# Kernel tuning notes

Hardware: AMD Instinct MI355X
Metric: run time of the kernel (lower is better)

## Reference

```python
import jax, jax.numpy as jnp
import numpy as np

B, N, D = 8, 1024, 512
H = 8
DH = D // H
EPS_DIST = 1e-8
EPS_LN = 1e-5


def _layer_norm(x, gamma, beta):
    mu = jnp.mean(x, axis=-1, keepdims=True)
    var = jnp.mean((x - mu) ** 2, axis=-1, keepdims=True)
    return (x - mu) * jax.lax.rsqrt(var + EPS_LN) * gamma + beta


def setup_inputs() -> dict:
    key = jax.random.key(0)
    ks = jax.random.split(key, 6)
    scale = 1.0 / np.sqrt(D)
    inp = {
        "x": jax.random.normal(ks[0], (B, N, D), dtype=jnp.float32),
        "Wq": jax.random.normal(ks[1], (D, D), dtype=jnp.float32) * scale,
        "Wk": jax.random.normal(ks[2], (D, D), dtype=jnp.float32) * scale,
        "Wv": jax.random.normal(ks[3], (D, D), dtype=jnp.float32) * scale,
        "Wo": jax.random.normal(ks[4], (D, D), dtype=jnp.float32) * scale,
        "bq": jnp.zeros((D,), jnp.float32),
        "bk": jnp.zeros((D,), jnp.float32),
        "bv": jnp.zeros((D,), jnp.float32),
        "bo": jnp.zeros((D,), jnp.float32),
        "ln1_g": jnp.ones((D,), jnp.float32),
        "ln1_b": jnp.zeros((D,), jnp.float32),
        "ln2_g": jnp.ones((D,), jnp.float32),
        "ln2_b": jnp.zeros((D,), jnp.float32),
    }
    return inp


def reference(x, Wq, bq, Wk, bk, Wv, bv, Wo, bo, ln1_g, ln1_b, ln2_g, ln2_b):
    residual = x
    h = _layer_norm(x, ln1_g, ln1_b)  # pre-norm

    def heads(t):
        # [B,N,D] -> [B,H,N,DH]
        return t.reshape(B, N, H, DH).transpose(0, 2, 1, 3)

    q = heads(h @ Wq + bq)
    k = heads(h @ Wk + bk)
    v = heads(h @ Wv + bv)

    # Euclidean pairwise distance via ||q||^2 + ||k||^2 - 2 q.k expansion
    q_sq = jnp.sum(q * q, axis=-1)[..., :, None]      # [B,H,N,1]
    k_sq = jnp.sum(k * k, axis=-1)[..., None, :]      # [B,H,1,N]
    qk = jnp.einsum("bhnd,bhmd->bhnm", q, k)          # [B,H,N,N]
    d2 = jnp.maximum(q_sq + k_sq - 2.0 * qk, 0.0)
    dist = jnp.sqrt(d2 + EPS_DIST)

    # distance -> attention score: smaller distance = higher attention
    attn = jax.nn.softmax(-dist, axis=-1)             # [B,H,N,N]

    out = jnp.einsum("bhnm,bhmd->bhnd", attn, v)      # [B,H,N,DH]
    out = out.transpose(0, 2, 1, 3).reshape(B, N, D)
    out = out @ Wo + bo

    y = residual + out
    y = _layer_norm(y, ln2_g, ln2_b)
    return y
```

## Files before the change

kernel.cpp:

```cpp
#include <hip/hip_runtime.h>
#include <math.h>

typedef __attribute__((ext_vector_type(8))) short short8;
typedef __attribute__((ext_vector_type(4))) float f32x4;
typedef __attribute__((ext_vector_type(2))) unsigned uint2v;

constexpr int B  = 8;
constexpr int N  = 1024;
constexpr int D  = 512;
constexpr int H  = 8;
constexpr int DH = 64;
constexpr int M_ROWS = 8192;
constexpr float EPS_DIST = 1e-8f;
constexpr float EPS_LN   = 1e-5f;

__device__ inline unsigned short bfbits(float f) {
    union { float f; unsigned u; } v; v.f = f;
    unsigned r = v.u + 0x7fffu + ((v.u >> 16) & 1u);
    return (unsigned short)(r >> 16);
}
__device__ inline float bf2f(unsigned short s) {
    union { unsigned u; float f; } v; v.u = ((unsigned)s) << 16; return v.f;
}

__device__ inline void async_ld16(unsigned short* lds, const unsigned short* g) {
    __builtin_amdgcn_global_load_lds(
        (const __attribute__((address_space(1))) unsigned int*)(g),
        (__attribute__((address_space(3))) unsigned int*)(lds),
        16, 0, 0);
}

__global__ __launch_bounds__(256) void prep_kernel(const float* __restrict__ Wq,
                                                   const float* __restrict__ Wk,
                                                   const float* __restrict__ Wv,
                                                   const float* __restrict__ Wo,
                                                   unsigned short* __restrict__ WtAll,
                                                   const float* __restrict__ x,
                                                   const float* __restrict__ ln1_g,
                                                   const float* __restrict__ ln1_b,
                                                   unsigned short* __restrict__ h_bf) {
    const int bxg = blockIdx.x;
    if (bxg < 256) {
        int sub = bxg >> 6;
        const float* W = sub == 0 ? Wq : sub == 1 ? Wk : sub == 2 ? Wv : Wo;
        unsigned short* Wt = WtAll + (size_t)sub * 262144;
        int t = (bxg & 63) * 256 + threadIdx.x;
        int tn = t & 127, tk = t >> 7;
        int k = tk * 4, n = tn * 4;
        float4 r0 = *(const float4*)&W[(size_t)(k + 0) * 512 + n];
        float4 r1 = *(const float4*)&W[(size_t)(k + 1) * 512 + n];
        float4 r2 = *(const float4*)&W[(size_t)(k + 2) * 512 + n];
        float4 r3 = *(const float4*)&W[(size_t)(k + 3) * 512 + n];
        ushort4 c;
        c.x = bfbits(r0.x); c.y = bfbits(r1.x); c.z = bfbits(r2.x); c.w = bfbits(r3.x);
        *(ushort4*)&Wt[(size_t)(n + 0) * 512 + k] = c;
        c.x = bfbits(r0.y); c.y = bfbits(r1.y); c.z = bfbits(r2.y); c.w = bfbits(r3.y);
        *(ushort4*)&Wt[(size_t)(n + 1) * 512 + k] = c;
        c.x = bfbits(r0.z); c.y = bfbits(r1.z); c.z = bfbits(r2.z); c.w = bfbits(r3.z);
        *(ushort4*)&Wt[(size_t)(n + 2) * 512 + k] = c;
        c.x = bfbits(r0.w); c.y = bfbits(r1.w); c.z = bfbits(r2.w); c.w = bfbits(r3.w);
        *(ushort4*)&Wt[(size_t)(n + 3) * 512 + k] = c;
    } else {
        const int w = threadIdx.x >> 6, lane = threadIdx.x & 63;
        const int row = (bxg - 256) * 4 + w;
        const float4* xr = (const float4*)(x + (size_t)row * D);
        float4 a = xr[lane], b2 = xr[lane + 64];
        float s = a.x + a.y + a.z + a.w + b2.x + b2.y + b2.z + b2.w;
        #pragma unroll
        for (int o = 1; o < 64; o <<= 1) s += __shfl_xor(s, o, 64);
        const float mu = s * (1.0f / 512.0f);
        float d0 = a.x - mu, d1 = a.y - mu, d2 = a.z - mu, d3 = a.w - mu;
        float e0 = b2.x - mu, e1 = b2.y - mu, e2 = b2.z - mu, e3 = b2.w - mu;
        float vs = d0*d0 + d1*d1 + d2*d2 + d3*d3 + e0*e0 + e1*e1 + e2*e2 + e3*e3;
        #pragma unroll
        for (int o = 1; o < 64; o <<= 1) vs += __shfl_xor(vs, o, 64);
        const float rstd = rsqrtf(vs * (1.0f / 512.0f) + EPS_LN);
        const float4* g4 = (const float4*)ln1_g;
        const float4* b4 = (const float4*)ln1_b;
        float4 ga = g4[lane], gb = g4[lane + 64];
        float4 ba = b4[lane], bb = b4[lane + 64];
        ushort4 u;
        u.x = bfbits(d0 * rstd * ga.x + ba.x);
        u.y = bfbits(d1 * rstd * ga.y + ba.y);
        u.z = bfbits(d2 * rstd * ga.z + ba.z);
        u.w = bfbits(d3 * rstd * ga.w + ba.w);
        *(ushort4*)&h_bf[(size_t)row * 512 + lane * 4] = u;
        u.x = bfbits(e0 * rstd * gb.x + bb.x);
        u.y = bfbits(e1 * rstd * gb.y + bb.y);
        u.z = bfbits(e2 * rstd * gb.z + bb.z);
        u.w = bfbits(e3 * rstd * gb.w + bb.w);
        *(ushort4*)&h_bf[(size_t)row * 512 + 256 + lane * 4] = u;
    }
}

__global__ __launch_bounds__(256) void ln2_kernel(const unsigned short* __restrict__ y0,
                                                  const float* __restrict__ res,
                                                  const float* __restrict__ gamma,
                                                  const float* __restrict__ beta,
                                                  float* __restrict__ out) {
    const int w = threadIdx.x >> 6, lane = threadIdx.x & 63;
    const int row = blockIdx.x * 4 + w;
    const ushort4* y4 = (const ushort4*)(y0 + (size_t)row * D);
    const float4*  r4 = (const float4*)(res + (size_t)row * D);
    ushort4 ya = y4[lane], yb = y4[lane + 64];
    float4  ra = r4[lane], rb = r4[lane + 64];
    float v0 = bf2f(ya.x) + ra.x, v1 = bf2f(ya.y) + ra.y;
    float v2 = bf2f(ya.z) + ra.z, v3 = bf2f(ya.w) + ra.w;
    float v4 = bf2f(yb.x) + rb.x, v5 = bf2f(yb.y) + rb.y;
    float v6 = bf2f(yb.z) + rb.z, v7 = bf2f(yb.w) + rb.w;
    float s = v0 + v1 + v2 + v3 + v4 + v5 + v6 + v7;
    #pragma unroll
    for (int o = 1; o < 64; o <<= 1) s += __shfl_xor(s, o, 64);
    const float mu = s * (1.0f / 512.0f);
    v0 -= mu; v1 -= mu; v2 -= mu; v3 -= mu;
    v4 -= mu; v5 -= mu; v6 -= mu; v7 -= mu;
    float vs = v0*v0 + v1*v1 + v2*v2 + v3*v3 + v4*v4 + v5*v5 + v6*v6 + v7*v7;
    #pragma unroll
    for (int o = 1; o < 64; o <<= 1) vs += __shfl_xor(vs, o, 64);
    const float rstd = rsqrtf(vs * (1.0f / 512.0f) + EPS_LN);
    const float4* g4 = (const float4*)gamma;
    const float4* b4 = (const float4*)beta;
    float4 ga = g4[lane], gb = g4[lane + 64];
    float4 ba = b4[lane], bb = b4[lane + 64];
    float4 o1, o2;
    o1.x = v0 * rstd * ga.x + ba.x; o1.y = v1 * rstd * ga.y + ba.y;
    o1.z = v2 * rstd * ga.z + ba.z; o1.w = v3 * rstd * ga.w + ba.w;
    o2.x = v4 * rstd * gb.x + bb.x; o2.y = v5 * rstd * gb.y + bb.y;
    o2.z = v6 * rstd * gb.z + bb.z; o2.w = v7 * rstd * gb.w + bb.w;
    float4* orow = (float4*)(out + (size_t)row * D);
    orow[lane]      = o1;
    orow[lane + 64] = o2;
}

template <int MODE, int MT>
__global__ __launch_bounds__(256) void gemm128(const unsigned short* __restrict__ A,
                                               const unsigned short* __restrict__ Wt,
                                               const float* __restrict__ bias0,
                                               const float* __restrict__ bias1,
                                               const float* __restrict__ bias2,
                                               void* __restrict__ o0,
                                               unsigned short* __restrict__ Ko,
                                               unsigned short* __restrict__ Vo,
                                               float* __restrict__ sq0,
                                               float* __restrict__ sq1) {
    constexpr int RB = M_ROWS / MT;
    constexpr int NI = MT / 32;
    constexpr int ASZ = MT * 64, BSZ = 128 * 64;
    constexpr int SMSZ = (MODE == 1) ? ((ASZ + BSZ > 18432) ? ASZ + BSZ : 18432)
                                     : (ASZ + BSZ);
    __shared__ unsigned short smem[SMSZ];
    unsigned short* As = smem;
    unsigned short* Bs = smem + ASZ;

    const int id = blockIdx.x;
    const int by = id & (RB - 1), bx = id / RB;
    const int tid = threadIdx.x;
    const int lane = tid & 63, wv = tid >> 6;
    const int quad = lane >> 4, l15 = lane & 15;
    const int row0 = by * MT, col0 = bx * 128;
    const int wm = (wv & 1) * (MT / 2), wn = (wv >> 1) * 64;

    f32x4 acc[NI][4];
    #pragma unroll
    for (int i = 0; i < NI; ++i)
        #pragma unroll
        for (int j = 0; j < 4; ++j) acc[i][j] = (f32x4){0.f, 0.f, 0.f, 0.f};

    const unsigned short* Ag = A  + (size_t)row0 * 512;
    const unsigned short* Bg = Wt + (size_t)col0 * 512;

    for (int k0 = 0; k0 < 512; k0 += 64) {
        __syncthreads();
        #pragma unroll
        for (int c = 0; c < ASZ / 2048; ++c) {
            int fu = c * 2048 + tid * 8;
            int r = fu >> 6, ko = fu & 63;
            async_ld16(As + fu, Ag + (size_t)r * 512 + k0 + ko);
        }
        #pragma unroll
        for (int c = 0; c < BSZ / 2048; ++c) {
            int fu = c * 2048 + tid * 8;
            int r = fu >> 6, ko = fu & 63;
            async_ld16(Bs + fu, Bg + (size_t)r * 512 + k0 + ko);
        }
        __syncthreads();

        #pragma unroll
        for (int ks = 0; ks < 2; ++ks) {
            short8 af[NI], bf[4];
            #pragma unroll
            for (int i = 0; i < NI; ++i)
                af[i] = *(const short8*)&As[(wm + i * 16 + l15) * 64 + ks * 32 + quad * 8];
            #pragma unroll
            for (int j = 0; j < 4; ++j)
                bf[j] = *(const short8*)&Bs[(wn + j * 16 + l15) * 64 + ks * 32 + quad * 8];
            #pragma unroll
            for (int i = 0; i < NI; ++i)
                #pragma unroll
                for (int j = 0; j < 4; ++j)
                    acc[i][j] = __builtin_amdgcn_mfma_f32_16x16x32_bf16(af[i], bf[j], acc[i][j], 0, 0, 0);
        }
    }

    if (MODE == 0) {
        unsigned short* C = (unsigned short*)o0;
        #pragma unroll
        for (int i = 0; i < NI; ++i)
            #pragma unroll
            for (int j = 0; j < 4; ++j) {
                int col = col0 + wn + j * 16 + l15;
                float bv = bias0[col];
                #pragma unroll
                for (int r = 0; r < 4; ++r) {
                    int row = row0 + wm + i * 16 + quad * 4 + r;
                    C[(size_t)row * 512 + col] = bfbits(acc[i][j][r] + bv);
                }
            }
    } else {
        const int colg = col0 + wn;
        const int seg = colg >> 9;
        const int hh = (colg & 511) >> 6;
        const float* bias = seg == 0 ? bias0 : seg == 1 ? bias1 : bias2;

        __syncthreads();
        unsigned short* T = smem + wv * 4608;

        if (seg < 2) {
            unsigned short* dst = seg == 0 ? (unsigned short*)o0 : Ko;
            float* sq = seg == 0 ? sq0 : sq1;
            #pragma unroll
            for (int i = 0; i < NI; ++i) {
                const int m0 = row0 + wm + i * 16 + quad * 4;
                float ss[4] = {0.f, 0.f, 0.f, 0.f};
                #pragma unroll
                for (int j = 0; j < 4; ++j) {
                    float bvj = bias[hh * 64 + j * 16 + l15];
                    #pragma unroll
                    for (int r = 0; r < 4; ++r) {
                        float v = acc[i][j][r] + bvj;
                        unsigned short ub = bfbits(v);
                        float vr = bf2f(ub);
                        ss[r] += vr * vr;
                        T[(i * 16 + quad * 4 + r) * 72 + j * 16 + l15] = ub;
                    }
                }
                #pragma unroll
                for (int r = 0; r < 4; ++r) {
                    float s = ss[r];
                    s += __shfl_xor(s, 1, 64);
                    s += __shfl_xor(s, 2, 64);
                    s += __shfl_xor(s, 4, 64);
                    s += __shfl_xor(s, 8, 64);
                    if (l15 == 0) {
                        int m = m0 + r;
                        sq[(size_t)((m >> 10) * 8 + hh) * 1024 + (m & 1023)] = s;
                    }
                }
            }
            const int b_ = (row0 + wm) >> 10;
            const int nbase = (row0 + wm) & 1023;
            unsigned short* Dg = dst + ((size_t)((b_ * 8 + hh) * 1024 + nbase)) * 64;
            #pragma unroll
            for (int it = 0; it < 8; ++it) {
                int ml = it * 8 + (lane >> 3);
                int dl = (lane & 7) * 8;
                uint4 v = *(const uint4*)&T[ml * 72 + dl];
                *(uint4*)&Dg[(size_t)ml * 64 + dl] = v;
            }
        } else {
            #pragma unroll
            for (int i = 0; i < NI; ++i)
                #pragma unroll
                for (int j = 0; j < 4; ++j) {
                    float bvj = bias[hh * 64 + j * 16 + l15];
                    ushort4 pk;
                    pk.x = bfbits(acc[i][j][0] + bvj);
                    pk.y = bfbits(acc[i][j][1] + bvj);
                    pk.z = bfbits(acc[i][j][2] + bvj);
                    pk.w = bfbits(acc[i][j][3] + bvj);
                    *(ushort4*)&T[(j * 16 + l15) * 72 + i * 16 + quad * 4] = pk;
                }
            const int b_ = (row0 + wm) >> 10;
            const int nbase = (row0 + wm) & 1023;
            unsigned short* Vg = Vo + ((size_t)((b_ * 8 + hh) * 64)) * 1024 + nbase;
            #pragma unroll
            for (int it = 0; it < 8; ++it) {
                int dl = it * 8 + (lane >> 3);
                int nl = (lane & 7) * 8;
                uint4 v = *(const uint4*)&T[dl * 72 + nl];
                *(uint4*)&Vg[(size_t)dl * 1024 + nl] = v;
            }
        }
    }
}

__global__ __launch_bounds__(256, 2) void attn_kernel(const unsigned short* __restrict__ Q,
                                                      const unsigned short* __restrict__ K,
                                                      const unsigned short* __restrict__ Vt,
                                                      const float* __restrict__ qsq,
                                                      const float* __restrict__ ksq,
                                                      unsigned short* __restrict__ O) {
    __shared__ unsigned short smem[2 * 4096 + 2 * 4096 + 256];
    unsigned short* KsB = smem;
    unsigned short* VsB = smem + 8192;
    float* ksq_s = (float*)(smem + 16384);

    const int id = blockIdx.x;
    const int bh = id & 63, qb = id >> 6;
    const int q0 = qb * 128;
    const int tid = threadIdx.x;
    const int lane = tid & 63, w = tid >> 6;
    const int quad = lane >> 4, l15 = lane & 15;
    const int b_ = bh >> 3, h_ = bh & 7;

    const unsigned short* Qb = Q  + (size_t)bh * N * DH;
    const unsigned short* Kb = K  + (size_t)bh * N * DH;
    const unsigned short* Vb = Vt + (size_t)bh * DH * N;

    short8 qf[2][2];
    #pragma unroll
    for (int qh = 0; qh < 2; ++qh) {
        const unsigned short* qp = Qb + (size_t)(q0 + w * 32 + qh * 16 + l15) * 64 + quad * 8;
        qf[qh][0] = *(const short8*)qp;
        qf[qh][1] = *(const short8*)(qp + 32);
        unsigned* qw = (unsigned*)&qf[qh][0];
        #pragma unroll
        for (int j = 0; j < 8; ++j) qw[j] = (qw[j] ^ 0x80008000u) + 0x00800080u;
    }
    float qe[2];
    qe[0] = qsq[bh * N + q0 + w * 32 + l15] + EPS_DIST;
    qe[1] = qsq[bh * N + q0 + w * 32 + 16 + l15] + EPS_DIST;

    const short8 onesf = {0x3F80, 0x3F80, 0x3F80, 0x3F80, 0x3F80, 0x3F80, 0x3F80, 0x3F80};

    f32x4 oacc[2][4];
    f32x4 dsum[2];
    #pragma unroll
    for (int qh = 0; qh < 2; ++qh) {
        dsum[qh] = (f32x4){0.f, 0.f, 0.f, 0.f};
        #pragma unroll
        for (int dt = 0; dt < 4; ++dt) oacc[qh][dt] = (f32x4){0.f, 0.f, 0.f, 0.f};
    }

    const int srow = tid >> 3;
    const int scol = ((tid & 7) * 8) ^ ((srow & 7) << 3);

    #pragma unroll
    for (int c = 0; c < 2; ++c) {
        const int e = c * 2048 + tid * 8;
        const int row = srow + c * 32;
        async_ld16(KsB + e, Kb + (size_t)row * 64 + scol);
        async_ld16(VsB + e, Vb + (size_t)row * N + scol);
    }
    if (tid < 64) ksq_s[tid] = ksq[bh * N + tid];
    __syncthreads();

    for (int kt = 0; kt < 16; ++kt) {
        const int cur = kt & 1;
        float ksreg = 0.f;
        if (kt < 15) {
            const int t64 = (kt + 1) * 64;
            #pragma unroll
            for (int c = 0; c < 2; ++c) {
                const int e = (cur ^ 1) * 4096 + c * 2048 + tid * 8;
                const int row = (c * 2048 + tid * 8) >> 6;
                const int cg = ((tid & 7) * 8) ^ ((row & 7) << 3);
                async_ld16(KsB + e, Kb + (size_t)(t64 + row) * 64 + cg);
                async_ld16(VsB + e, Vb + (size_t)row * N + t64 + cg);
            }
            if (tid < 64) ksreg = ksq[bh * N + t64 + tid];
        }

        #pragma unroll
        for (int kc = 0; kc < 2; ++kc) {
            unsigned Wp[2][2][2];
            #pragma unroll
            for (int kh = 0; kh < 2; ++kh) {
                const int kb = kc * 2 + kh;
                const int krow = kb * 16 + l15;
                const int ksw = (krow & 7) << 3;
                const unsigned short* kbase = KsB + cur * 4096 + krow * 64;
                short8 kf0 = *(const short8*)&kbase[(quad * 8) ^ ksw];
                short8 kf1 = *(const short8*)&kbase[(32 + quad * 8) ^ ksw];
                f32x4 ks2 = *(const f32x4*)&ksq_s[cur * 64 + kb * 16 + quad * 4];
                #pragma unroll
                for (int qh = 0; qh < 2; ++qh) {
                    f32x4 sa;
                    #pragma unroll
                    for (int r = 0; r < 4; ++r) sa[r] = ks2[r] + qe[qh];
                    sa = __builtin_amdgcn_mfma_f32_16x16x32_bf16(kf0, qf[qh][0], sa, 0, 0, 0);
                    sa = __builtin_amdgcn_mfma_f32_16x16x32_bf16(kf1, qf[qh][1], sa, 0, 0, 0);
                    float pr[4];
                    #pragma unroll
                    for (int r = 0; r < 4; ++r) {
                        float d2 = fmaxf(sa[r], EPS_DIST);
                        pr[r] = __expf(-__builtin_amdgcn_sqrtf(d2));
                    }
                    union { float f; unsigned u; } u0, u1, u2, u3;
                    u0.f = pr[0]; u1.f = pr[1]; u2.f = pr[2]; u3.f = pr[3];
                    Wp[qh][kh][0] = __builtin_amdgcn_perm(u1.u, u0.u, 0x07060302u);
                    Wp[qh][kh][1] = __builtin_amdgcn_perm(u3.u, u2.u, 0x07060302u);
                }
            }

            short8 vf[4];
            #pragma unroll
            for (int dt = 0; dt < 4; ++dt) {
                const int vrow = dt * 16 + l15;
                vf[dt] = *(const short8*)&VsB[cur * 4096 + vrow * 64 +
                                              ((kc * 32 + quad * 8) ^ ((vrow & 7) << 3))];
            }

            #pragma unroll
            for (int qh = 0; qh < 2; ++qh) {
                uint2v ya = __builtin_amdgcn_permlane32_swap(Wp[qh][0][0], Wp[qh][1][0], false, false);
                uint2v za = __builtin_amdgcn_permlane16_swap(ya.x, ya.y, false, false);
                uint2v yb = __builtin_amdgcn_permlane32_swap(Wp[qh][0][1], Wp[qh][1][1], false, false);
                uint2v zb = __builtin_amdgcn_permlane16_swap(yb.x, yb.y, false, false);
                union { unsigned wds[4]; short8 s; } pu;
                pu.wds[0] = za.x; pu.wds[1] = zb.x; pu.wds[2] = za.y; pu.wds[3] = zb.y;
                short8 pf = pu.s;
                dsum[qh] = __builtin_amdgcn_mfma_f32_16x16x32_bf16(pf, onesf, dsum[qh], 0, 0, 0);
                #pragma unroll
                for (int dt = 0; dt < 4; ++dt)
                    oacc[qh][dt] = __builtin_amdgcn_mfma_f32_16x16x32_bf16(pf, vf[dt], oacc[qh][dt], 0, 0, 0);
            }
        }

        if (kt < 15 && tid < 64) ksq_s[(cur ^ 1) * 64 + tid] = ksreg;
        __syncthreads();
    }

    unsigned short* T3 = smem + w * 2304;
    #pragma unroll
    for (int qh = 0; qh < 2; ++qh) {
        f32x4 rv;
        #pragma unroll
        for (int r = 0; r < 4; ++r) rv[r] = __builtin_amdgcn_rcpf(dsum[qh][r]);
        #pragma unroll
        for (int dt = 0; dt < 4; ++dt)
            #pragma unroll
            for (int r = 0; r < 4; ++r)
                T3[(qh * 16 + quad * 4 + r) * 72 + dt * 16 + l15] =
                    bfbits(oacc[qh][dt][r] * rv[r]);
    }
    unsigned short* Og = O + ((size_t)(b_ * N + q0 + w * 32) * D) + h_ * DH;
    #pragma unroll
    for (int it = 0; it < 4; ++it) {
        int ml = it * 8 + (lane >> 3);
        int dl = (lane & 7) * 8;
        uint4 v = *(const uint4*)&T3[ml * 72 + dl];
        *(uint4*)&Og[(size_t)ml * D + dl] = v;
    }
}

extern "C" void kernel_launch(void* const* d_in, const int* in_sizes, int n_in,
                              void* d_out, int out_size, void* d_ws, size_t ws_size,
                              hipStream_t stream) {
    const float* x     = (const float*)d_in[0];
    const float* Wq    = (const float*)d_in[1];
    const float* Wk    = (const float*)d_in[2];
    const float* Wv    = (const float*)d_in[3];
    const float* Wo    = (const float*)d_in[4];
    const float* bq    = (const float*)d_in[5];
    const float* bk    = (const float*)d_in[6];
    const float* bv    = (const float*)d_in[7];
    const float* bo    = (const float*)d_in[8];
    const float* ln1_g = (const float*)d_in[9];
    const float* ln1_b = (const float*)d_in[10];
    const float* ln2_g = (const float*)d_in[11];
    const float* ln2_b = (const float*)d_in[12];
    float* out = (float*)d_out;

    unsigned short* WtAll = (unsigned short*)d_ws;
    unsigned short* h_bf  = WtAll + 4 * 262144;
    unsigned short* Qb    = h_bf + 4194304;
    unsigned short* Kb    = Qb + 4194304;
    unsigned short* Vtg   = Kb + 4194304;
    unsigned short* Ob    = Vtg + 4194304;
    unsigned short* Y0    = Ob + 4194304;
    float* qsq = (float*)(Y0 + 4194304);
    float* ksq = qsq + 65536;

    prep_kernel<<<256 + M_ROWS / 4, 256, 0, stream>>>(Wq, Wk, Wv, Wo, WtAll,
                                                      x, ln1_g, ln1_b, h_bf);

    gemm128<1, 128><<<768, 256, 0, stream>>>(h_bf, WtAll, bq, bk, bv,
                                             Qb, Kb, Vtg, qsq, ksq);

    attn_kernel<<<512, 256, 0, stream>>>(Qb, Kb, Vtg, qsq, ksq, Ob);

    gemm128<0, 64><<<512, 256, 0, stream>>>(Ob, WtAll + 3 * 262144, bo,
                                            nullptr, nullptr, Y0,
                                            nullptr, nullptr, nullptr, nullptr);

    ln2_kernel<<<M_ROWS / 4, 256, 0, stream>>>(Y0, x, ln2_g, ln2_b, out);
}
```

Measured before the change: 174.0 us.

## Halve attention query tile to 64 rows and launch twice as many blocks

The attention kernel now gives each block 64 query rows instead of 128, so each wave handles 16 rows. The grid doubles to 1024 blocks and launch bounds target 4 blocks per CU to raise occupancy and fill the GPU better. The cost is that K/V tiles are loaded from global into LDS twice as often relative to compute, which lowers reuse. The weight-transpose thread mapping in prep is also swapped so neighbouring threads step along k instead of n, which changes its memory access pattern.

```diff
diff --git a/kernel.cpp b/kernel.cpp
--- a/kernel.cpp
+++ b/kernel.cpp
@@ -45,7 +45,7 @@
         const float* W = sub == 0 ? Wq : sub == 1 ? Wk : sub == 2 ? Wv : Wo;
         unsigned short* Wt = WtAll + (size_t)sub * 262144;
         int t = (bxg & 63) * 256 + threadIdx.x;
-        int tn = t & 127, tk = t >> 7;
+        int tk = t & 127, tn = t >> 7;
         int k = tk * 4, n = tn * 4;
         float4 r0 = *(const float4*)&W[(size_t)(k + 0) * 512 + n];
         float4 r1 = *(const float4*)&W[(size_t)(k + 1) * 512 + n];
@@ -294,7 +294,7 @@
     }
 }
 
-__global__ __launch_bounds__(256, 2) void attn_kernel(const unsigned short* __restrict__ Q,
+__global__ __launch_bounds__(256, 4) void attn_kernel(const unsigned short* __restrict__ Q,
                                                       const unsigned short* __restrict__ K,
                                                       const unsigned short* __restrict__ Vt,
                                                       const float* __restrict__ qsq,
@@ -307,7 +307,7 @@
 
     const int id = blockIdx.x;
     const int bh = id & 63, qb = id >> 6;
-    const int q0 = qb * 128;
+    const int q0 = qb * 64;
     const int tid = threadIdx.x;
     const int lane = tid & 63, w = tid >> 6;
     const int quad = lane >> 4, l15 = lane & 15;
@@ -317,30 +317,23 @@
     const unsigned short* Kb = K  + (size_t)bh * N * DH;
     const unsigned short* Vb = Vt + (size_t)bh * DH * N;
 
-    short8 qf[2][2];
-    #pragma unroll
-    for (int qh = 0; qh < 2; ++qh) {
-        const unsigned short* qp = Qb + (size_t)(q0 + w * 32 + qh * 16 + l15) * 64 + quad * 8;
-        qf[qh][0] = *(const short8*)qp;
-        qf[qh][1] = *(const short8*)(qp + 32);
-        unsigned* qw = (unsigned*)&qf[qh][0];
+    short8 qf[2];
+    {
+        const unsigned short* qp = Qb + (size_t)(q0 + w * 16 + l15) * 64 + quad * 8;
+        qf[0] = *(const short8*)qp;
+        qf[1] = *(const short8*)(qp + 32);
+        unsigned* qw = (unsigned*)&qf[0];
         #pragma unroll
         for (int j = 0; j < 8; ++j) qw[j] = (qw[j] ^ 0x80008000u) + 0x00800080u;
     }
-    float qe[2];
-    qe[0] = qsq[bh * N + q0 + w * 32 + l15] + EPS_DIST;
-    qe[1] = qsq[bh * N + q0 + w * 32 + 16 + l15] + EPS_DIST;
+    const float qe = qsq[bh * N + q0 + w * 16 + l15] + EPS_DIST;
 
     const short8 onesf = {0x3F80, 0x3F80, 0x3F80, 0x3F80, 0x3F80, 0x3F80, 0x3F80, 0x3F80};
 
-    f32x4 oacc[2][4];
-    f32x4 dsum[2];
-    #pragma unroll
-    for (int qh = 0; qh < 2; ++qh) {
-        dsum[qh] = (f32x4){0.f, 0.f, 0.f, 0.f};
-        #pragma unroll
-        for (int dt = 0; dt < 4; ++dt) oacc[qh][dt] = (f32x4){0.f, 0.f, 0.f, 0.f};
-    }
+    f32x4 oacc[4];
+    f32x4 dsum = (f32x4){0.f, 0.f, 0.f, 0.f};
+    #pragma unroll
+    for (int dt = 0; dt < 4; ++dt) oacc[dt] = (f32x4){0.f, 0.f, 0.f, 0.f};
 
     const int srow = tid >> 3;
     const int scol = ((tid & 7) * 8) ^ ((srow & 7) << 3);
@@ -363,7 +356,7 @@
             #pragma unroll
             for (int c = 0; c < 2; ++c) {
                 const int e = (cur ^ 1) * 4096 + c * 2048 + tid * 8;
-                const int row = (c * 2048 + tid * 8) >> 6;
+                const int row = srow + c * 32;
                 const int cg = ((tid & 7) * 8) ^ ((row & 7) << 3);
                 async_ld16(KsB + e, Kb + (size_t)(t64 + row) * 64 + cg);
                 async_ld16(VsB + e, Vb + (size_t)row * N + t64 + cg);
@@ -373,7 +366,7 @@
 
         #pragma unroll
         for (int kc = 0; kc < 2; ++kc) {
-            unsigned Wp[2][2][2];
+            unsigned Wp[2][2];
             #pragma unroll
             for (int kh = 0; kh < 2; ++kh) {
                 const int kb = kc * 2 + kh;
@@ -383,24 +376,21 @@
                 short8 kf0 = *(const short8*)&kbase[(quad * 8) ^ ksw];
                 short8 kf1 = *(const short8*)&kbase[(32 + quad * 8) ^ ksw];
                 f32x4 ks2 = *(const f32x4*)&ksq_s[cur * 64 + kb * 16 + quad * 4];
-                #pragma unroll
-                for (int qh = 0; qh < 2; ++qh) {
-                    f32x4 sa;
-                    #pragma unroll
-                    for (int r = 0; r < 4; ++r) sa[r] = ks2[r] + qe[qh];
-                    sa = __builtin_amdgcn_mfma_f32_16x16x32_bf16(kf0, qf[qh][0], sa, 0, 0, 0);
-                    sa = __builtin_amdgcn_mfma_f32_16x16x32_bf16(kf1, qf[qh][1], sa, 0, 0, 0);
-                    float pr[4];
-                    #pragma unroll
-                    for (int r = 0; r < 4; ++r) {
-                        float d2 = fmaxf(sa[r], EPS_DIST);
-                        pr[r] = __expf(-__builtin_amdgcn_sqrtf(d2));
-                    }
-                    union { float f; unsigned u; } u0, u1, u2, u3;
-                    u0.f = pr[0]; u1.f = pr[1]; u2.f = pr[2]; u3.f = pr[3];
-                    Wp[qh][kh][0] = __builtin_amdgcn_perm(u1.u, u0.u, 0x07060302u);
-                    Wp[qh][kh][1] = __builtin_amdgcn_perm(u3.u, u2.u, 0x07060302u);
+                f32x4 sa;
+                #pragma unroll
+                for (int r = 0; r < 4; ++r) sa[r] = ks2[r] + qe;
+                sa = __builtin_amdgcn_mfma_f32_16x16x32_bf16(kf0, qf[0], sa, 0, 0, 0);
+                sa = __builtin_amdgcn_mfma_f32_16x16x32_bf16(kf1, qf[1], sa, 0, 0, 0);
+                float pr[4];
+                #pragma unroll
+                for (int r = 0; r < 4; ++r) {
+                    float d2 = fmaxf(sa[r], EPS_DIST);
+                    pr[r] = __expf(-__builtin_amdgcn_sqrtf(d2));
                 }
+                union { float f; unsigned u; } u0, u1, u2, u3;
+                u0.f = pr[0]; u1.f = pr[1]; u2.f = pr[2]; u3.f = pr[3];
+                Wp[kh][0] = __builtin_amdgcn_perm(u1.u, u0.u, 0x07060302u);
+                Wp[kh][1] = __builtin_amdgcn_perm(u3.u, u2.u, 0x07060302u);
             }
 
             short8 vf[4];
@@ -411,19 +401,18 @@
                                               ((kc * 32 + quad * 8) ^ ((vrow & 7) << 3))];
             }
 
-            #pragma unroll
-            for (int qh = 0; qh < 2; ++qh) {
-                uint2v ya = __builtin_amdgcn_permlane32_swap(Wp[qh][0][0], Wp[qh][1][0], false, false);
+            {
+                uint2v ya = __builtin_amdgcn_permlane32_swap(Wp[0][0], Wp[1][0], false, false);
                 uint2v za = __builtin_amdgcn_permlane16_swap(ya.x, ya.y, false, false);
-                uint2v yb = __builtin_amdgcn_permlane32_swap(Wp[qh][0][1], Wp[qh][1][1], false, false);
+                uint2v yb = __builtin_amdgcn_permlane32_swap(Wp[0][1], Wp[1][1], false, false);
                 uint2v zb = __builtin_amdgcn_permlane16_swap(yb.x, yb.y, false, false);
                 union { unsigned wds[4]; short8 s; } pu;
                 pu.wds[0] = za.x; pu.wds[1] = zb.x; pu.wds[2] = za.y; pu.wds[3] = zb.y;
                 short8 pf = pu.s;
-                dsum[qh] = __builtin_amdgcn_mfma_f32_16x16x32_bf16(pf, onesf, dsum[qh], 0, 0, 0);
+                dsum = __builtin_amdgcn_mfma_f32_16x16x32_bf16(pf, onesf, dsum, 0, 0, 0);
                 #pragma unroll
                 for (int dt = 0; dt < 4; ++dt)
-                    oacc[qh][dt] = __builtin_amdgcn_mfma_f32_16x16x32_bf16(pf, vf[dt], oacc[qh][dt], 0, 0, 0);
+                    oacc[dt] = __builtin_amdgcn_mfma_f32_16x16x32_bf16(pf, vf[dt], oacc[dt], 0, 0, 0);
             }
         }
 
@@ -431,22 +420,21 @@
         __syncthreads();
     }
 
-    unsigned short* T3 = smem + w * 2304;
-    #pragma unroll
-    for (int qh = 0; qh < 2; ++qh) {
+    unsigned short* T3 = smem + w * 1152;
+    {
         f32x4 rv;
         #pragma unroll
-        for (int r = 0; r < 4; ++r) rv[r] = __builtin_amdgcn_rcpf(dsum[qh][r]);
+        for (int r = 0; r < 4; ++r) rv[r] = __builtin_amdgcn_rcpf(dsum[r]);
         #pragma unroll
         for (int dt = 0; dt < 4; ++dt)
             #pragma unroll
             for (int r = 0; r < 4; ++r)
-                T3[(qh * 16 + quad * 4 + r) * 72 + dt * 16 + l15] =
-                    bfbits(oacc[qh][dt][r] * rv[r]);
-    }
-    unsigned short* Og = O + ((size_t)(b_ * N + q0 + w * 32) * D) + h_ * DH;
-    #pragma unroll
-    for (int it = 0; it < 4; ++it) {
+                T3[(quad * 4 + r) * 72 + dt * 16 + l15] =
+                    bfbits(oacc[dt][r] * rv[r]);
+    }
+    unsigned short* Og = O + ((size_t)(b_ * N + q0 + w * 16) * D) + h_ * DH;
+    #pragma unroll
+    for (int it = 0; it < 2; ++it) {
         int ml = it * 8 + (lane >> 3);
         int dl = (lane & 7) * 8;
         uint4 v = *(const uint4*)&T3[ml * 72 + dl];
@@ -488,7 +476,7 @@
     gemm128<1, 128><<<768, 256, 0, stream>>>(h_bf, WtAll, bq, bk, bv,
                                              Qb, Kb, Vtg, qsq, ksq);
 
-    attn_kernel<<<512, 256, 0, stream>>>(Qb, Kb, Vtg, qsq, ksq, Ob);
+    attn_kernel<<<1024, 256, 0, stream>>>(Qb, Kb, Vtg, qsq, ksq, Ob);
 
     gemm128<0, 64><<<512, 256, 0, stream>>>(Ob, WtAll + 3 * 262144, bo,
                                             nullptr, nullptr, Y0,
```

Result: no change. 175.7 us (+1.0%).
